# Performance work log

Hardware: AMD Instinct MI355X
Metric: run time of the kernel (lower is better)

The kernel has to match this reference:

```python
import jax, jax.numpy as jnp
import numpy as np

LATENT = 256
OUT_CH = 1
K = 16
HEADS = 64


def _conv1x1(x, W, b):
    # x: [B, Cin, ...spatial], W: [Cout, Cin], b: [Cout]
    y = jnp.einsum('oc,bc...->bo...', W, x)
    return y + b.reshape((1, -1) + (1,) * (y.ndim - 2))


def _batch_gather(x, idx):
    # x: [B, C, N], idx: [B, Nq, K] -> [B, C, Nq, K]
    return jax.vmap(lambda xb, ib: xb[:, ib])(x, idx)


def setup_inputs() -> dict:
    key = jax.random.key(0)
    ks = jax.random.split(key, 16)
    B, N, NQ = 2, 10000, 10000
    inp = {
        'latents': jax.random.normal(ks[0], (B, LATENT, N), jnp.float32),
        'pts': jax.random.normal(ks[1], (B, 3, N), jnp.float32),
        'pts_query': jax.random.normal(ks[2], (B, 3, NQ), jnp.float32),
        'proj_ids': jax.random.randint(ks[3], (B, NQ, K), 0, N, jnp.int64),
    }
    def lin(k, o, i):
        s = 1.0 / np.sqrt(i)
        k1, k2 = jax.random.split(k)
        return (jax.random.uniform(k1, (o, i), jnp.float32, -s, s),
                jax.random.uniform(k2, (o,), jnp.float32, -s, s))
    inp['W1'], inp['b1'] = lin(ks[4], LATENT, LATENT + 3)
    inp['W2'], inp['b2'] = lin(ks[5], LATENT, LATENT)
    inp['W3'], inp['b3'] = lin(ks[6], LATENT, LATENT)
    inp['Wq'], inp['bq'] = lin(ks[7], HEADS, LATENT)
    inp['Wv'], inp['bv'] = lin(ks[8], LATENT, LATENT)
    inp['W8'], inp['b8'] = lin(ks[9], OUT_CH, LATENT)
    return inp


def reference(latents, pts, pts_query, proj_ids,
              W1, b1, W2, b2, W3, b3, Wq, bq, Wv, bv, W8, b8):
    # gather neighbor latents and points: [B, C, Nq, K], [B, 3, Nq, K]
    x = _batch_gather(latents, proj_ids)
    npts = _batch_gather(pts, proj_ids)
    rel = pts_query[:, :, :, None] - npts          # [B, 3, Nq, K]
    x = jnp.concatenate([x, rel], axis=1)          # [B, C+3, Nq, K]
    x = jax.nn.relu(_conv1x1(x, W1, b1))
    x = jax.nn.relu(_conv1x1(x, W2, b2))
    x = jax.nn.relu(_conv1x1(x, W3, b3))
    query = _conv1x1(x, Wq, bq)                    # [B, 64, Nq, K]
    value = _conv1x1(x, Wv, bv)                    # [B, C, Nq, K]
    attention = jax.nn.softmax(query, axis=-1).mean(axis=1)  # [B, Nq, K]
    # weighted sum over K neighbors: [B, Nq, C] -> [B, C, Nq]
    x = jnp.einsum('bnk,bcnk->bcn', attention, value)
    x = _conv1x1(x, W8, b8)                        # [B, out_ch, Nq]
    return x
```

## Files before the change

### kernel.cpp

```cpp
#include <hip/hip_runtime.h>
#include <cstdint>
#include <cstddef>


#define NLAT 256
#define KNB 16
#define QB 4
#define MROWS 64
#define ROWB 576

typedef float    f32x4 __attribute__((ext_vector_type(4)));
typedef _Float16 f16x8 __attribute__((ext_vector_type(8)));
typedef _Float16 f16x4 __attribute__((ext_vector_type(4)));

struct Smem {
  unsigned char buf[MROWS * ROWB];
  float Sp[4][MROWS];
  float Sv[MROWS];
  int sidx[MROWS];
  int is64;
};

__device__ __forceinline__ void layer_mfma(
    unsigned char* __restrict__ buf, const unsigned short* __restrict__ Wp,
    const float* __restrict__ bias, const float* __restrict__ W1f,
    int lane, int wave, bool relu)
{
  const int lm = lane & 15, lk = lane >> 4, rk = lm & 7;
  const char* bp0 = (const char*)buf + lm * 576 + ((2 * lk) ^ rk) * 8;
  const char* bp1 = (const char*)buf + lm * 576 + ((2 * lk + 1) ^ rk) * 8;
  const char* wbase = (const char*)Wp + lk * 4096 + (wave * 64 + lm) * 16;

  f32x4 acc[4][4];
#pragma unroll
  for (int i = 0; i < 4; ++i)
#pragma unroll
    for (int j = 0; j < 4; ++j) acc[i][j] = (f32x4){0.f, 0.f, 0.f, 0.f};

#pragma unroll
  for (int ks = 0; ks < 8; ++ks) {
    const char* wk = wbase + ks * 16384;
    f16x8 a[4], bf[4];
#pragma unroll
    for (int ct = 0; ct < 4; ++ct)
      a[ct] = *(const f16x8*)(wk + ct * 256);
#pragma unroll
    for (int mt = 0; mt < 4; ++mt) {
      f16x4 lo = *(const f16x4*)(bp0 + mt * 9216 + ks * 64);
      f16x4 hi = *(const f16x4*)(bp1 + mt * 9216 + ks * 64);
      bf[mt] = __builtin_shufflevector(lo, hi, 0, 1, 2, 3, 4, 5, 6, 7);
    }
#pragma unroll
    for (int ct = 0; ct < 4; ++ct)
#pragma unroll
      for (int mt = 0; mt < 4; ++mt)
        acc[ct][mt] = __builtin_amdgcn_mfma_f32_16x16x32_f16(a[ct], bf[mt], acc[ct][mt], 0, 0, 0);
  }
  if (W1f) {
    f16x8 a[4], bf[4];
#pragma unroll
    for (int ct = 0; ct < 4; ++ct) {
      f16x8 v = {0, 0, 0, 0, 0, 0, 0, 0};
      if (lk == 0) {
        const int ch = wave * 64 + ct * 16 + lm;
        const float* wt = W1f + (size_t)ch * 259 + 256;
        v[0] = (_Float16)wt[0]; v[1] = (_Float16)wt[1]; v[2] = (_Float16)wt[2];
      }
      a[ct] = v;
    }
#pragma unroll
    for (int mt = 0; mt < 4; ++mt) {
      f16x4 lo = *(const f16x4*)(bp0 + mt * 9216 + 512);
      f16x4 hi = *(const f16x4*)(bp1 + mt * 9216 + 512);
      bf[mt] = __builtin_shufflevector(lo, hi, 0, 1, 2, 3, 4, 5, 6, 7);
    }
#pragma unroll
    for (int ct = 0; ct < 4; ++ct)
#pragma unroll
      for (int mt = 0; mt < 4; ++mt)
        acc[ct][mt] = __builtin_amdgcn_mfma_f32_16x16x32_f16(a[ct], bf[mt], acc[ct][mt], 0, 0, 0);
  }
  __syncthreads();
  char* we0 = (char*)buf + lm * 576 + wave * 128 + (lk ^ rk) * 8;
  char* we1 = (char*)buf + lm * 576 + wave * 128 + ((4 + lk) ^ rk) * 8;
#pragma unroll
  for (int ct = 0; ct < 4; ++ct) {
    const int ch0 = wave * 64 + ct * 16 + lk * 4;
    const float4 bs = *(const float4*)(bias + ch0);
    const float bb[4] = {bs.x, bs.y, bs.z, bs.w};
    char* web = ((ct & 1) ? we1 : we0) + (ct >> 1) * 64;
#pragma unroll
    for (int mt = 0; mt < 4; ++mt) {
      f16x4 v;
#pragma unroll
      for (int r = 0; r < 4; ++r) {
        float x = acc[ct][mt][r] + bb[r];
        if (relu) x = fmaxf(x, 0.f);
        v[r] = (_Float16)x;
      }
      *(f16x4*)(web + mt * 9216) = v;
    }
  }
}

extern "C" __global__ __launch_bounds__(256, 3)
void interp_mfma(const float* __restrict__ latents,
                 const float* __restrict__ pts,
                 const float* __restrict__ ptsq,
                 const void*  __restrict__ proj,
                 const unsigned short* __restrict__ Lt_u,
                 const float* __restrict__ W1f,
                 const unsigned short* __restrict__ W1p,
                 const unsigned short* __restrict__ W2p,
                 const unsigned short* __restrict__ W3p,
                 const unsigned short* __restrict__ Wqh,
                 const float* __restrict__ b1, const float* __restrict__ b2,
                 const float* __restrict__ b3, const float* __restrict__ bq,
                 const float* __restrict__ wv8, const float* __restrict__ c0p,
                 float* __restrict__ out,
                 int N, int NQ, int use_lt)
{
  __shared__ Smem sm;
  const int tid = threadIdx.x;
  const int bid = blockIdx.x;
  const int lane = tid & 63, wave = tid >> 6;
  const int lm = lane & 15, lk = lane >> 4, rk = lm & 7;

  if (tid == 0) {
    const int* p = (const int*)proj;
    int z = 1;
    for (int i = 0; i < 64; ++i) z &= (p[2 * i + 1] == 0);
    sm.is64 = z;
  }
  __syncthreads();
  if (tid < MROWS) {
    long long g = (long long)bid * QB + (tid >> 4);
    long long base = g * KNB + (tid & 15);
    sm.sidx[tid] = sm.is64 ? (int)((const long long*)proj)[base]
                           : ((const int*)proj)[base];
  }
  __syncthreads();

  {
    const int row = tid >> 2, part = tid & 3, rg = row & 7;
    const int id = sm.sidx[row];
    const long long g = (long long)bid * QB + (row >> 4);
    const int b = (int)(g / NQ);
    char* g0 = (char*)sm.buf + row * 576 + ((2 * part) ^ rg) * 8;
    char* g1 = (char*)sm.buf + row * 576 + ((2 * part + 1) ^ rg) * 8;
    if (use_lt) {
      const _Float16* src = (const _Float16*)Lt_u + ((size_t)b * N + id) * NLAT + part * 8;
#pragma unroll
      for (int jj = 0; jj < 8; ++jj) {
        f16x8 v = *(const f16x8*)(src + jj * 32);
        f16x4 vl = {v[0], v[1], v[2], v[3]}, vh = {v[4], v[5], v[6], v[7]};
        *(f16x4*)(g0 + jj * 64) = vl;
        *(f16x4*)(g1 + jj * 64) = vh;
      }
    } else {
      for (int jj = 0; jj < 8; ++jj) {
        f16x4 vl, vh;
#pragma unroll
        for (int e = 0; e < 4; ++e) {
          vl[e] = (_Float16)latents[((size_t)b * NLAT + (2 * part + 8 * jj) * 4 + e) * N + id];
          vh[e] = (_Float16)latents[((size_t)b * NLAT + (2 * part + 1 + 8 * jj) * 4 + e) * N + id];
        }
        *(f16x4*)(g0 + jj * 64) = vl;
        *(f16x4*)(g1 + jj * 64) = vh;
      }
    }
    const f16x4 z = {0, 0, 0, 0};
    f16x4 v0 = z;
    if (part == 0) {
      const int nq = (int)(g - (long long)b * NQ);
#pragma unroll
      for (int j = 0; j < 3; ++j)
        v0[j] = (_Float16)(ptsq[((size_t)b * 3 + j) * NQ + nq]
                         - pts[((size_t)b * 3 + j) * N + id]);
    }
    *(f16x4*)((char*)sm.buf + row * 576 + 512 + ((2 * part) ^ rg) * 8) = v0;
    *(f16x4*)((char*)sm.buf + row * 576 + 512 + ((2 * part + 1) ^ rg) * 8) = z;
  }
  __syncthreads();

  layer_mfma(sm.buf, W1p, b1, W1f, lane, wave, true);
  __syncthreads();
  layer_mfma(sm.buf, W2p, b2, nullptr, lane, wave, true);
  __syncthreads();
  layer_mfma(sm.buf, W3p, b3, nullptr, lane, wave, true);
  __syncthreads();

  const char* bp0 = (const char*)sm.buf + lm * 576 + ((2 * lk) ^ rk) * 8;
  const char* bp1 = (const char*)sm.buf + lm * 576 + ((2 * lk + 1) ^ rk) * 8;
  f32x4 qacc[4];
#pragma unroll
  for (int mt = 0; mt < 4; ++mt) qacc[mt] = (f32x4){0.f, 0.f, 0.f, 0.f};
  {
    const char* wqb = (const char*)Wqh + (wave * 16 + lm) * 512 + lk * 16;
#pragma unroll
    for (int ks = 0; ks < 8; ++ks) {
      f16x8 a = *(const f16x8*)(wqb + ks * 64);
#pragma unroll
      for (int mt = 0; mt < 4; ++mt) {
        f16x4 lo = *(const f16x4*)(bp0 + mt * 9216 + ks * 64);
        f16x4 hi = *(const f16x4*)(bp1 + mt * 9216 + ks * 64);
        f16x8 bf = __builtin_shufflevector(lo, hi, 0, 1, 2, 3, 4, 5, 6, 7);
        qacc[mt] = __builtin_amdgcn_mfma_f32_16x16x32_f16(a, bf, qacc[mt], 0, 0, 0);
      }
    }
  }
  {
    const char* sp0 = bp0 + wave * 9216;
    const char* sp1 = bp1 + wave * 9216;
    float sacc = 0.f;
#pragma unroll
    for (int cc = 0; cc < 8; ++cc) {
      f16x4 lo = *(const f16x4*)(sp0 + cc * 64);
      f16x4 hi = *(const f16x4*)(sp1 + cc * 64);
      const int c = cc * 4 + lk;
      const float4 w0 = *(const float4*)(wv8 + c * 8);
      const float4 w1 = *(const float4*)(wv8 + c * 8 + 4);
      sacc += (float)lo[0] * w0.x + (float)lo[1] * w0.y
            + (float)lo[2] * w0.z + (float)lo[3] * w0.w;
      sacc += (float)hi[0] * w1.x + (float)hi[1] * w1.y
            + (float)hi[2] * w1.z + (float)hi[3] * w1.w;
    }
    sacc += __shfl_xor(sacc, 16);
    sacc += __shfl_xor(sacc, 32);
    if (lk == 0) sm.Sv[wave * 16 + lm] = sacc;
  }

  {
    float bqv[4];
#pragma unroll
    for (int r = 0; r < 4; ++r) bqv[r] = bq[wave * 16 + lk * 4 + r];
#pragma unroll
    for (int mt = 0; mt < 4; ++mt) {
      float sw = 0.f;
#pragma unroll
      for (int r = 0; r < 4; ++r) {
        const float qv = qacc[mt][r] + bqv[r];
        float mx = qv;
#pragma unroll
        for (int msk = 1; msk < 16; msk <<= 1) mx = fmaxf(mx, __shfl_xor(mx, msk));
        const float e = __expf(qv - mx);
        float s = e;
#pragma unroll
        for (int msk = 1; msk < 16; msk <<= 1) s += __shfl_xor(s, msk);
        sw += e / s;
      }
      sw += __shfl_xor(sw, 16);
      sw += __shfl_xor(sw, 32);
      if (lk == 0) sm.Sp[wave][mt * 16 + lm] = sw;
    }
  }
  __syncthreads();

  {
    const int m = wave * 16 + lm;
    const float a = (sm.Sp[0][m] + sm.Sp[1][m] + sm.Sp[2][m] + sm.Sp[3][m]) * (1.f / 64.f);
    float val = a * sm.Sv[m];
#pragma unroll
    for (int msk = 1; msk < 16; msk <<= 1) val += __shfl_xor(val, msk);
    if (lane == 0) out[(long long)bid * QB + wave] = val + c0p[0];
  }
}

extern "C" __global__ void prep_w(const float* __restrict__ W1, const float* __restrict__ W2,
                                  const float* __restrict__ W3, const float* __restrict__ Wq,
                                  const float* __restrict__ Wv, const float* __restrict__ W8,
                                  const float* __restrict__ bv, const float* __restrict__ b8,
                                  unsigned short* W1p, unsigned short* W2p,
                                  unsigned short* W3p, unsigned short* Wqh,
                                  float* wv8, float* c0) {
  const int t = blockIdx.x * 256 + threadIdx.x;
  union { _Float16 h; unsigned short u; } cv;
  if (t < 65536) {
    const int ch = t >> 8, k = t & 255;
    const int dst = (((k >> 3) << 8) + ch) * 8 + (k & 7);
    cv.h = (_Float16)W1[(size_t)ch * 259 + k]; W1p[dst] = cv.u;
    cv.h = (_Float16)W2[t]; W2p[dst] = cv.u;
    cv.h = (_Float16)W3[t]; W3p[dst] = cv.u;
  }
  if (t < 16384) { cv.h = (_Float16)Wq[t]; Wqh[t] = cv.u; }
  if (t < 256) {
    float s = 0.f;
    for (int o = 0; o < 256; ++o) s += Wv[(size_t)o * 256 + t] * W8[o];
    wv8[t] = s;
  }
  if (t == 0) {
    float s = 0.f;
    for (int o = 0; o < 256; ++o) s += bv[o] * W8[o];
    c0[0] = s + b8[0];
  }
}

extern "C" __global__ void transp(const float* __restrict__ latents,
                                  unsigned short* __restrict__ Lt, int N) {
  __shared__ unsigned short tile[256][68];
  const int b = blockIdx.y, n0 = blockIdx.x * 64, tid = threadIdx.x;
  const int nl = tid & 63;
  union { _Float16 h; unsigned short u; } cv;
  for (int c = tid >> 6; c < 256; c += 4) {
    const int n = n0 + nl;
    float v = (n < N) ? latents[((size_t)b * NLAT + c) * N + n] : 0.f;
    cv.h = (_Float16)v;
    tile[c][nl] = cv.u;
  }
  __syncthreads();
  const int nr = tid >> 2, cg = (tid & 3) * 64;
  const int n = n0 + nr;
  if (n < N) {
    for (int cc = 0; cc < 64; cc += 8) {
      f16x8 v;
#pragma unroll
      for (int j = 0; j < 8; ++j) {
        union { unsigned short u; _Float16 h; } bk;
        bk.u = tile[cg + cc + j][nr];
        v[j] = bk.h;
      }
      *(f16x8*)((_Float16*)Lt + ((size_t)b * N + n) * NLAT + cg + cc) = v;
    }
  }
}

extern "C" void kernel_launch(void* const* d_in, const int* in_sizes, int n_in,
                              void* d_out, int out_size, void* d_ws, size_t ws_size,
                              hipStream_t stream) {
  (void)n_in; (void)out_size;
  const float* latents = (const float*)d_in[0];
  const float* pts     = (const float*)d_in[1];
  const float* ptsq    = (const float*)d_in[2];
  const void*  proj    = d_in[3];
  const float* W1 = (const float*)d_in[4];  const float* b1 = (const float*)d_in[5];
  const float* W2 = (const float*)d_in[6];  const float* b2 = (const float*)d_in[7];
  const float* W3 = (const float*)d_in[8];  const float* b3 = (const float*)d_in[9];
  const float* Wq = (const float*)d_in[10]; const float* bq = (const float*)d_in[11];
  const float* Wv = (const float*)d_in[12]; const float* bv = (const float*)d_in[13];
  const float* W8 = (const float*)d_in[14]; const float* b8 = (const float*)d_in[15];
  float* out = (float*)d_out;

  const int B  = 2;
  const int N  = in_sizes[1] / (3 * B);
  const int NQ = in_sizes[2] / (3 * B);

  size_t off = 0;
  auto alloc = [&](size_t bytes) -> char* {
    char* p = (char*)d_ws + off;
    off += (bytes + 255) & ~(size_t)255;
    return p;
  };
  unsigned short* W1p = (unsigned short*)alloc(65536 * 2);
  unsigned short* W2p = (unsigned short*)alloc(65536 * 2);
  unsigned short* W3p = (unsigned short*)alloc(65536 * 2);
  unsigned short* Wqh = (unsigned short*)alloc(16384 * 2);
  float* wv8 = (float*)alloc(256 * 4);
  float* c0  = (float*)alloc(4);
  const size_t lt_bytes = (size_t)B * N * NLAT * 2;
  unsigned short* Lt = (unsigned short*)((char*)d_ws + off);
  const int use_lt = (off + lt_bytes <= ws_size) ? 1 : 0;

  hipLaunchKernelGGL(prep_w, dim3(256), dim3(256), 0, stream,
                     W1, W2, W3, Wq, Wv, W8, bv, b8, W1p, W2p, W3p, Wqh, wv8, c0);
  if (use_lt)
    hipLaunchKernelGGL(transp, dim3((N + 63) / 64, B), dim3(256), 0, stream,
                       latents, Lt, N);
  const int nblocks = (B * NQ + QB - 1) / QB;
  hipLaunchKernelGGL(interp_mfma, dim3(nblocks), dim3(256), 0, stream,
                     latents, pts, ptsq, proj, Lt, W1, W1p, W2p, W3p, Wqh,
                     b1, b2, b3, bq, wv8, c0, out, N, NQ, use_lt);
}
```

Baseline: 218.9 us.

## Switch MLP layers to 32x32x16 MFMA with padded row layout

```diff
diff --git a/kernel.cpp b/kernel.cpp
--- a/kernel.cpp
+++ b/kernel.cpp
@@ -7,11 +7,12 @@
 #define KNB 16
 #define QB 4
 #define MROWS 64
-#define ROWB 576
-
-typedef float    f32x4 __attribute__((ext_vector_type(4)));
-typedef _Float16 f16x8 __attribute__((ext_vector_type(8)));
-typedef _Float16 f16x4 __attribute__((ext_vector_type(4)));
+#define ROWB 560
+
+typedef float    f32x4  __attribute__((ext_vector_type(4)));
+typedef float    f32x16 __attribute__((ext_vector_type(16)));
+typedef _Float16 f16x8  __attribute__((ext_vector_type(8)));
+typedef _Float16 f16x4  __attribute__((ext_vector_type(4)));
 
 struct Smem {
   unsigned char buf[MROWS * ROWB];
@@ -21,89 +22,81 @@
   int is64;
 };
 
-__device__ __forceinline__ void layer_mfma(
+__device__ __forceinline__ void layer_mfma32(
     unsigned char* __restrict__ buf, const unsigned short* __restrict__ Wp,
     const float* __restrict__ bias, const float* __restrict__ W1f,
     int lane, int wave, bool relu)
 {
-  const int lm = lane & 15, lk = lane >> 4, rk = lm & 7;
-  const char* bp0 = (const char*)buf + lm * 576 + ((2 * lk) ^ rk) * 8;
-  const char* bp1 = (const char*)buf + lm * 576 + ((2 * lk + 1) ^ rk) * 8;
-  const char* wbase = (const char*)Wp + lk * 4096 + (wave * 64 + lm) * 16;
-
-  f32x4 acc[4][4];
-#pragma unroll
-  for (int i = 0; i < 4; ++i)
-#pragma unroll
-    for (int j = 0; j < 4; ++j) acc[i][j] = (f32x4){0.f, 0.f, 0.f, 0.f};
-
-#pragma unroll
-  for (int ks = 0; ks < 8; ++ks) {
-    const char* wk = wbase + ks * 16384;
-    f16x8 a[4], bf[4];
-#pragma unroll
-    for (int ct = 0; ct < 4; ++ct)
-      a[ct] = *(const f16x8*)(wk + ct * 256);
-#pragma unroll
-    for (int mt = 0; mt < 4; ++mt) {
-      f16x4 lo = *(const f16x4*)(bp0 + mt * 9216 + ks * 64);
-      f16x4 hi = *(const f16x4*)(bp1 + mt * 9216 + ks * 64);
-      bf[mt] = __builtin_shufflevector(lo, hi, 0, 1, 2, 3, 4, 5, 6, 7);
-    }
-#pragma unroll
-    for (int ct = 0; ct < 4; ++ct)
-#pragma unroll
-      for (int mt = 0; mt < 4; ++mt)
-        acc[ct][mt] = __builtin_amdgcn_mfma_f32_16x16x32_f16(a[ct], bf[mt], acc[ct][mt], 0, 0, 0);
+  const int lm32 = lane & 31, h = lane >> 5;
+  const char* bp = (const char*)buf + lm32 * 560 + h * 16;
+  const char* wbase = (const char*)Wp + (wave * 2) * 1024 + lm32 * 32 + h * 16;
+
+  f32x16 acc[2][2];
+#pragma unroll
+  for (int i = 0; i < 2; ++i)
+#pragma unroll
+    for (int j = 0; j < 2; ++j) acc[i][j] = (f32x16)(0.f);
+
+#pragma unroll
+  for (int ks = 0; ks < 16; ++ks) {
+    f16x8 a[2], b[2];
+#pragma unroll
+    for (int ct = 0; ct < 2; ++ct)
+      a[ct] = *(const f16x8*)(wbase + ks * 8192 + ct * 1024);
+#pragma unroll
+    for (int mt = 0; mt < 2; ++mt)
+      b[mt] = *(const f16x8*)(bp + mt * 17920 + ks * 32);
+#pragma unroll
+    for (int ct = 0; ct < 2; ++ct)
+#pragma unroll
+      for (int mt = 0; mt < 2; ++mt)
+        acc[ct][mt] = __builtin_amdgcn_mfma_f32_32x32x16_f16(a[ct], b[mt], acc[ct][mt], 0, 0, 0);
   }
   if (W1f) {
-    f16x8 a[4], bf[4];
-#pragma unroll
-    for (int ct = 0; ct < 4; ++ct) {
+    f16x8 a[2], b[2];
+#pragma unroll
+    for (int ct = 0; ct < 2; ++ct) {
       f16x8 v = {0, 0, 0, 0, 0, 0, 0, 0};
-      if (lk == 0) {
-        const int ch = wave * 64 + ct * 16 + lm;
+      if (h == 0) {
+        const int ch = (wave * 2 + ct) * 32 + lm32;
         const float* wt = W1f + (size_t)ch * 259 + 256;
         v[0] = (_Float16)wt[0]; v[1] = (_Float16)wt[1]; v[2] = (_Float16)wt[2];
       }
       a[ct] = v;
     }
 #pragma unroll
-    for (int mt = 0; mt < 4; ++mt) {
-      f16x4 lo = *(const f16x4*)(bp0 + mt * 9216 + 512);
-      f16x4 hi = *(const f16x4*)(bp1 + mt * 9216 + 512);
-      bf[mt] = __builtin_shufflevector(lo, hi, 0, 1, 2, 3, 4, 5, 6, 7);
-    }
-#pragma unroll
-    for (int ct = 0; ct < 4; ++ct)
-#pragma unroll
-      for (int mt = 0; mt < 4; ++mt)
-        acc[ct][mt] = __builtin_amdgcn_mfma_f32_16x16x32_f16(a[ct], bf[mt], acc[ct][mt], 0, 0, 0);
-  }
-  __syncthreads();
-  char* we0 = (char*)buf + lm * 576 + wave * 128 + (lk ^ rk) * 8;
-  char* we1 = (char*)buf + lm * 576 + wave * 128 + ((4 + lk) ^ rk) * 8;
-#pragma unroll
-  for (int ct = 0; ct < 4; ++ct) {
-    const int ch0 = wave * 64 + ct * 16 + lk * 4;
-    const float4 bs = *(const float4*)(bias + ch0);
-    const float bb[4] = {bs.x, bs.y, bs.z, bs.w};
-    char* web = ((ct & 1) ? we1 : we0) + (ct >> 1) * 64;
-#pragma unroll
-    for (int mt = 0; mt < 4; ++mt) {
-      f16x4 v;
-#pragma unroll
-      for (int r = 0; r < 4; ++r) {
-        float x = acc[ct][mt][r] + bb[r];
-        if (relu) x = fmaxf(x, 0.f);
-        v[r] = (_Float16)x;
-      }
-      *(f16x4*)(web + mt * 9216) = v;
-    }
-  }
-}
-
-extern "C" __global__ __launch_bounds__(256, 3)
+    for (int mt = 0; mt < 2; ++mt)
+      b[mt] = *(const f16x8*)(bp + mt * 17920 + 512);
+#pragma unroll
+    for (int ct = 0; ct < 2; ++ct)
+#pragma unroll
+      for (int mt = 0; mt < 2; ++mt)
+        acc[ct][mt] = __builtin_amdgcn_mfma_f32_32x32x16_f16(a[ct], b[mt], acc[ct][mt], 0, 0, 0);
+  }
+  __syncthreads();
+#pragma unroll
+  for (int ct = 0; ct < 2; ++ct) {
+#pragma unroll
+    for (int q = 0; q < 4; ++q) {
+      const int ch0 = (wave * 2 + ct) * 32 + q * 8 + h * 4;
+      const float4 bs = *(const float4*)(bias + ch0);
+      const float bb[4] = {bs.x, bs.y, bs.z, bs.w};
+#pragma unroll
+      for (int mt = 0; mt < 2; ++mt) {
+        f16x4 v;
+#pragma unroll
+        for (int j = 0; j < 4; ++j) {
+          float x = acc[ct][mt][q * 4 + j] + bb[j];
+          if (relu) x = fmaxf(x, 0.f);
+          v[j] = (_Float16)x;
+        }
+        *(f16x4*)((char*)buf + (mt * 32 + lm32) * 560 + ch0 * 2) = v;
+      }
+    }
+  }
+}
+
+extern "C" __global__ __launch_bounds__(256, 4)
 void interp_mfma(const float* __restrict__ latents,
                  const float* __restrict__ pts,
                  const float* __restrict__ ptsq,
@@ -124,7 +117,7 @@
   const int tid = threadIdx.x;
   const int bid = blockIdx.x;
   const int lane = tid & 63, wave = tid >> 6;
-  const int lm = lane & 15, lk = lane >> 4, rk = lm & 7;
+  const int lm = lane & 15, lk = lane >> 4;
 
   if (tid == 0) {
     const int* p = (const int*)proj;
@@ -142,56 +135,47 @@
   __syncthreads();
 
   {
-    const int row = tid >> 2, part = tid & 3, rg = row & 7;
+    const int row = tid & 63, part = tid >> 6;
     const int id = sm.sidx[row];
     const long long g = (long long)bid * QB + (row >> 4);
     const int b = (int)(g / NQ);
-    char* g0 = (char*)sm.buf + row * 576 + ((2 * part) ^ rg) * 8;
-    char* g1 = (char*)sm.buf + row * 576 + ((2 * part + 1) ^ rg) * 8;
+    char* dst = (char*)sm.buf + row * 560 + part * 128;
     if (use_lt) {
-      const _Float16* src = (const _Float16*)Lt_u + ((size_t)b * N + id) * NLAT + part * 8;
-#pragma unroll
-      for (int jj = 0; jj < 8; ++jj) {
-        f16x8 v = *(const f16x8*)(src + jj * 32);
-        f16x4 vl = {v[0], v[1], v[2], v[3]}, vh = {v[4], v[5], v[6], v[7]};
-        *(f16x4*)(g0 + jj * 64) = vl;
-        *(f16x4*)(g1 + jj * 64) = vh;
-      }
+      const _Float16* src = (const _Float16*)Lt_u + ((size_t)b * N + id) * NLAT + part * 64;
+#pragma unroll
+      for (int cc = 0; cc < 8; ++cc)
+        *(f16x8*)(dst + cc * 16) = *(const f16x8*)(src + cc * 8);
     } else {
-      for (int jj = 0; jj < 8; ++jj) {
-        f16x4 vl, vh;
-#pragma unroll
-        for (int e = 0; e < 4; ++e) {
-          vl[e] = (_Float16)latents[((size_t)b * NLAT + (2 * part + 8 * jj) * 4 + e) * N + id];
-          vh[e] = (_Float16)latents[((size_t)b * NLAT + (2 * part + 1 + 8 * jj) * 4 + e) * N + id];
-        }
-        *(f16x4*)(g0 + jj * 64) = vl;
-        *(f16x4*)(g1 + jj * 64) = vh;
-      }
-    }
-    const f16x4 z = {0, 0, 0, 0};
-    f16x4 v0 = z;
+      for (int cc = 0; cc < 8; ++cc) {
+        f16x8 v;
+#pragma unroll
+        for (int e = 0; e < 8; ++e)
+          v[e] = (_Float16)latents[((size_t)b * NLAT + part * 64 + cc * 8 + e) * N + id];
+        *(f16x8*)(dst + cc * 16) = v;
+      }
+    }
     if (part == 0) {
       const int nq = (int)(g - (long long)b * NQ);
+      f16x8 v = {0, 0, 0, 0, 0, 0, 0, 0};
 #pragma unroll
       for (int j = 0; j < 3; ++j)
-        v0[j] = (_Float16)(ptsq[((size_t)b * 3 + j) * NQ + nq]
-                         - pts[((size_t)b * 3 + j) * N + id]);
-    }
-    *(f16x4*)((char*)sm.buf + row * 576 + 512 + ((2 * part) ^ rg) * 8) = v0;
-    *(f16x4*)((char*)sm.buf + row * 576 + 512 + ((2 * part + 1) ^ rg) * 8) = z;
-  }
-  __syncthreads();
-
-  layer_mfma(sm.buf, W1p, b1, W1f, lane, wave, true);
-  __syncthreads();
-  layer_mfma(sm.buf, W2p, b2, nullptr, lane, wave, true);
-  __syncthreads();
-  layer_mfma(sm.buf, W3p, b3, nullptr, lane, wave, true);
-  __syncthreads();
-
-  const char* bp0 = (const char*)sm.buf + lm * 576 + ((2 * lk) ^ rk) * 8;
-  const char* bp1 = (const char*)sm.buf + lm * 576 + ((2 * lk + 1) ^ rk) * 8;
+        v[j] = (_Float16)(ptsq[((size_t)b * 3 + j) * NQ + nq]
+                        - pts[((size_t)b * 3 + j) * N + id]);
+      const f16x8 z = {0, 0, 0, 0, 0, 0, 0, 0};
+      *(f16x8*)((char*)sm.buf + row * 560 + 512) = v;
+      *(f16x8*)((char*)sm.buf + row * 560 + 528) = z;
+    }
+  }
+  __syncthreads();
+
+  layer_mfma32(sm.buf, W1p, b1, W1f, lane, wave, true);
+  __syncthreads();
+  layer_mfma32(sm.buf, W2p, b2, nullptr, lane, wave, true);
+  __syncthreads();
+  layer_mfma32(sm.buf, W3p, b3, nullptr, lane, wave, true);
+  __syncthreads();
+
+  const char* bp16 = (const char*)sm.buf + lm * 560 + lk * 16;
   f32x4 qacc[4];
 #pragma unroll
   for (int mt = 0; mt < 4; ++mt) qacc[mt] = (f32x4){0.f, 0.f, 0.f, 0.f};
@@ -202,28 +186,24 @@
       f16x8 a = *(const f16x8*)(wqb + ks * 64);
 #pragma unroll
       for (int mt = 0; mt < 4; ++mt) {
-        f16x4 lo = *(const f16x4*)(bp0 + mt * 9216 + ks * 64);
-        f16x4 hi = *(const f16x4*)(bp1 + mt * 9216 + ks * 64);
-        f16x8 bf = __builtin_shufflevector(lo, hi, 0, 1, 2, 3, 4, 5, 6, 7);
+        f16x8 bf = *(const f16x8*)(bp16 + mt * 8960 + ks * 64);
         qacc[mt] = __builtin_amdgcn_mfma_f32_16x16x32_f16(a, bf, qacc[mt], 0, 0, 0);
       }
     }
   }
   {
-    const char* sp0 = bp0 + wave * 9216;
-    const char* sp1 = bp1 + wave * 9216;
+    const char* sp = (const char*)sm.buf + (wave * 16 + lm) * 560 + lk * 16;
     float sacc = 0.f;
 #pragma unroll
     for (int cc = 0; cc < 8; ++cc) {
-      f16x4 lo = *(const f16x4*)(sp0 + cc * 64);
-      f16x4 hi = *(const f16x4*)(sp1 + cc * 64);
-      const int c = cc * 4 + lk;
-      const float4 w0 = *(const float4*)(wv8 + c * 8);
-      const float4 w1 = *(const float4*)(wv8 + c * 8 + 4);
-      sacc += (float)lo[0] * w0.x + (float)lo[1] * w0.y
-            + (float)lo[2] * w0.z + (float)lo[3] * w0.w;
-      sacc += (float)hi[0] * w1.x + (float)hi[1] * w1.y
-            + (float)hi[2] * w1.z + (float)hi[3] * w1.w;
+      f16x8 v = *(const f16x8*)(sp + cc * 64);
+      const int k0 = cc * 32 + lk * 8;
+      const float4 w0 = *(const float4*)(wv8 + k0);
+      const float4 w1 = *(const float4*)(wv8 + k0 + 4);
+      sacc += (float)v[0] * w0.x + (float)v[1] * w0.y
+            + (float)v[2] * w0.z + (float)v[3] * w0.w;
+      sacc += (float)v[4] * w1.x + (float)v[5] * w1.y
+            + (float)v[6] * w1.z + (float)v[7] * w1.w;
     }
     sacc += __shfl_xor(sacc, 16);
     sacc += __shfl_xor(sacc, 32);
@@ -277,7 +257,7 @@
   union { _Float16 h; unsigned short u; } cv;
   if (t < 65536) {
     const int ch = t >> 8, k = t & 255;
-    const int dst = (((k >> 3) << 8) + ch) * 8 + (k & 7);
+    const int dst = (k >> 4) * 4096 + ch * 16 + ((k >> 3) & 1) * 8 + (k & 7);
     cv.h = (_Float16)W1[(size_t)ch * 259 + k]; W1p[dst] = cv.u;
     cv.h = (_Float16)W2[t]; W2p[dst] = cv.u;
     cv.h = (_Float16)W3[t]; W3p[dst] = cv.u;
```

Measured after the change: 219.5 us. No clear change (+0.3%).
